# Kernel tuning notes

Measured on AMD Instinct MI355X. Metric: run time of the kernel, lower is better.

Reference implementation:

```python
import jax, jax.numpy as jnp
import numpy as np
from jax import lax

B, T = 8192, 4096


def setup_inputs() -> dict:
    key = jax.random.key(0)
    ks = jax.random.split(key, 16)
    P = jax.random.uniform(ks[0], (B, T, 1), dtype=jnp.float32) * 10.0  # precipitation, mm
    lengths = jax.random.randint(ks[1], (B,), 1, T + 1, dtype=jnp.int32)
    initial_S = jax.random.uniform(ks[2], (4,), dtype=jnp.float32) * 20.0  # initial tank levels
    Area = jnp.array([100.0], dtype=jnp.float32)  # catchment area km^2
    baseflow = jnp.array([0.0], dtype=jnp.float32)  # unused by forward, kept for signature fidelity

    def u(k, lo, hi):
        return jax.random.uniform(k, (1,), dtype=jnp.float32) * (hi - lo) + lo

    params = {
        "outflow_rate_1_h1": u(ks[3], 0.05, 0.25),
        "outflow_rate_1_h2": u(ks[4], 0.05, 0.10),
        "height_1_h1": u(ks[5], 40.0, 60.0),
        "height_1_h2": u(ks[6], 0.0, 40.0),
        "inflow_rate_2": u(ks[7], 0.01, 0.30),
        "outflow_rate_2": u(ks[8], 0.005, 0.30),
        "height_2": u(ks[9], 0.0, 30.0),
        "inflow_rate_3": u(ks[10], 0.005, 0.20),
        "outflow_rate_3": u(ks[11], 0.005, 0.15),
        "height_3": u(ks[12], 0.0, 30.0),
        "inflow_rate_4": u(ks[13], 0.005, 0.10),
        "outflow_rate_4": u(ks[14], 0.0006, 0.10),
    }
    return {"P": P, "lengths": lengths, "initial_S": initial_S, "Area": Area,
            "baseflow": baseflow, **params}


def reference(P, lengths, initial_S, Area, baseflow,
              outflow_rate_1_h1, outflow_rate_1_h2, height_1_h1, height_1_h2,
              inflow_rate_2, outflow_rate_2, height_2,
              inflow_rate_3, outflow_rate_3, height_3,
              inflow_rate_4, outflow_rate_4):
    Pq = P[..., 0]                              # [B, T]
    b, t = Pq.shape
    # valid_mask[b, t] = (lengths[b] > t), as in pad_packed_sequence masking
    mask = (jnp.arange(t)[None, :] < lengths[:, None]).astype(Pq.dtype)  # [B, T]
    w_init = tuple(jnp.broadcast_to(initial_S[i], (b,)) for i in range(4))

    def step(carry, xs):
        w1, w2, w3, w4 = carry
        p, m = xs                               # [B] each
        # Tank 1: two side outlets + bottom percolation into tank 2
        of1h1 = jnp.maximum(outflow_rate_1_h1 * (w1 - height_1_h1 + p), 0.0) * m
        of1h2 = jnp.maximum(outflow_rate_1_h2 * (w1 - height_1_h2 + p), 0.0) * m
        of1 = (of1h1 + of1h2) * m
        out12 = jnp.maximum(inflow_rate_2 * (w1 + p), 0.0) * m
        w1 = w1 + (p - of1 - out12) * m
        # Tank 2
        of2 = jnp.maximum(outflow_rate_2 * (w2 + out12 - height_2), 0.0) * m
        out23 = jnp.maximum(inflow_rate_3 * (w2 + out12), 0.0) * m
        w2 = w2 + (out12 - of2 - out23) * m
        # Tank 3
        of3 = jnp.maximum(outflow_rate_3 * (w3 + out23 - height_3), 0.0) * m
        out34 = jnp.maximum(inflow_rate_4 * (w3 + out23), 0.0) * m
        w3 = w3 + (out23 - of3 - out34) * m
        # Tank 4 (deep baseflow tank)
        of4 = jnp.maximum(outflow_rate_4 * (w4 + out34), 0.0) * m
        w4 = w4 + (out34 - of4) * m
        total = (of1 + of2 + of3 + of4) * m
        return (w1, w2, w3, w4), total * Area / 3.6   # mm -> m^3/s conversion

    _, ys = lax.scan(step, w_init, (Pq.T, mask.T))    # ys: [T, B]
    return ys.T                                        # [B, T]
```

## Files before the change

kernel.cpp:

```cpp
#include <hip/hip_runtime.h>
#include <stdint.h>


__device__ __forceinline__ float quad_rot1(float x) {
    int xi = __builtin_bit_cast(int, x);
    int r = __builtin_amdgcn_update_dpp(xi, xi, 0x93, 0xF, 0xF, false);
    return __builtin_bit_cast(float, r);
}

__global__ __launch_bounds__(64)
void tank_kernel(
    const float* __restrict__ P,
    const int*   __restrict__ lengths,
    const float* __restrict__ S0,
    const float* __restrict__ AreaP,
    const float* __restrict__ p_r1h1, const float* __restrict__ p_r1h2,
    const float* __restrict__ p_h1h1, const float* __restrict__ p_h1h2,
    const float* __restrict__ p_ri2,  const float* __restrict__ p_ro2,
    const float* __restrict__ p_h2,
    const float* __restrict__ p_ri3,  const float* __restrict__ p_ro3,
    const float* __restrict__ p_h3,
    const float* __restrict__ p_ri4,  const float* __restrict__ p_ro4,
    float* __restrict__ Out,
    int B, int T)
{
    __shared__ float4 inbuf[2 * 256];
    __shared__ float4 outbuf[3 * 256];

    const int tid = threadIdx.x;
    const int g   = tid >> 2;
    const int k   = tid & 3;
    const int row = blockIdx.x * 16 + g;
    const int rowc = (row < B) ? row : (B - 1);
    const bool is0 = (k == 0);
    const bool is3 = (k == 3);
    const float zk = (k == 0) ? 0.0f : 1.0f;

    const float v_r1h1 = p_r1h1[0], v_r1h2 = p_r1h2[0];
    const float v_h11 = p_h1h1[0], v_h12 = p_h1h2[0];
    const float v_ri2 = p_ri2[0], v_ro2 = p_ro2[0], v_h2 = p_h2[0];
    const float v_ri3 = p_ri3[0], v_ro3 = p_ro3[0], v_h3 = p_h3[0];
    const float v_ri4 = p_ri4[0], v_ro4 = p_ro4[0];
    const float scale = AreaP[0] * (1.0f / 3.6f);

    float rA = v_ro4, kA = 0.0f, rB = 0.0f, kB = 0.0f, riN = 0.0f;
    if (k == 0) { rA = v_r1h1; kA = -v_r1h1 * v_h11; rB = v_r1h2; kB = -v_r1h2 * v_h12; riN = v_ri2; }
    else if (k == 1) { rA = v_ro2; kA = -v_ro2 * v_h2; riN = v_ri3; }
    else if (k == 2) { rA = v_ro3; kA = -v_ro3 * v_h3; riN = v_ri4; }

    float w = (k == 0) ? S0[0] : (k == 1) ? S0[1] : (k == 2) ? S0[2] : S0[3];

    int len = lengths[rowc];
    if (len > T) len = T;
    if (len < 0) len = 0;

    float fl0 = 0.0f, fl1 = 0.0f, fl2 = 0.0f, fl3 = 0.0f;
    float ps0 = 0.0f, ps1 = 0.0f, ps2 = 0.0f, ps3 = 0.0f;
    const int ntiles = T / 64;

#define HOP4(CX, CY, CZ, CW, FREEZE, hidx) do {                   \
        float r0_ = quad_rot1(fl0);                               \
        float r1_ = quad_rot1(fl1);                               \
        float r2_ = quad_rot1(fl2);                               \
        float r3_ = quad_rot1(fl3);                               \
        float q0_ = quad_rot1(ps0);                               \
        float q1_ = quad_rot1(ps1);                               \
        float q2_ = quad_rot1(ps2);                               \
        float q3_ = quad_rot1(ps3);                               \
        float i0_ = is0 ? (CX) : r0_;                             \
        float i1_ = is0 ? (CY) : r1_;                             \
        float i2_ = is0 ? (CZ) : r2_;                             \
        float i3_ = is0 ? (CW) : r3_;                             \
        float t_, a1_, a2_, e_, Y_, wn_;                          \
                                                      \
        t_  = w + i0_;                                            \
        a1_ = fmaxf(fmaf(rA, t_, kA), 0.0f);                      \
        a2_ = fmaxf(fmaf(rB, t_, kB), 0.0f);                      \
        e_  = fmaxf(t_, 0.0f);                                    \
        fl0 = riN * e_;                                           \
        Y_  = a1_ + a2_;                                          \
        wn_ = (t_ - fl0) - Y_;                                    \
        w = (FREEZE) ? (((hidx) >= k) ? wn_ : w) : wn_;           \
        ps0 = fmaf(q0_, zk, Y_);                                  \
                                                      \
        t_  = w + i1_;                                            \
        a1_ = fmaxf(fmaf(rA, t_, kA), 0.0f);                      \
        a2_ = fmaxf(fmaf(rB, t_, kB), 0.0f);                      \
        e_  = fmaxf(t_, 0.0f);                                    \
        fl1 = riN * e_;                                           \
        Y_  = a1_ + a2_;                                          \
        wn_ = (t_ - fl1) - Y_;                                    \
        w = (FREEZE) ? (((hidx) >= k) ? wn_ : w) : wn_;           \
        ps1 = fmaf(q1_, zk, Y_);                                  \
                                                      \
        t_  = w + i2_;                                            \
        a1_ = fmaxf(fmaf(rA, t_, kA), 0.0f);                      \
        a2_ = fmaxf(fmaf(rB, t_, kB), 0.0f);                      \
        e_  = fmaxf(t_, 0.0f);                                    \
        fl2 = riN * e_;                                           \
        Y_  = a1_ + a2_;                                          \
        wn_ = (t_ - fl2) - Y_;                                    \
        w = (FREEZE) ? (((hidx) >= k) ? wn_ : w) : wn_;           \
        ps2 = fmaf(q2_, zk, Y_);                                  \
                                                      \
        t_  = w + i3_;                                            \
        a1_ = fmaxf(fmaf(rA, t_, kA), 0.0f);                      \
        a2_ = fmaxf(fmaf(rB, t_, kB), 0.0f);                      \
        e_  = fmaxf(t_, 0.0f);                                    \
        fl3 = riN * e_;                                           \
        Y_  = a1_ + a2_;                                          \
        wn_ = (t_ - fl3) - Y_;                                    \
        w = (FREEZE) ? (((hidx) >= k) ? wn_ : w) : wn_;           \
        ps3 = fmaf(q3_, zk, Y_);                                  \
    } while (0)

#define STAGE_LOAD(mt) do {                                               \
        const float* src_ = P + (size_t)rowc * T + (mt) * 64;             \
        _Pragma("unroll")                                                 \
        for (int r = 0; r < 4; ++r)                                       \
            st[r] = *reinterpret_cast<const float4*>(src_ + (4 * r + k) * 4); \
    } while (0)

#define STAGE_LDS(ibp) do {                                  \
        _Pragma("unroll")                                    \
        for (int r = 0; r < 4; ++r)                          \
            (ibp)[g * 16 + ((4 * r + k) ^ g)] = st[r];       \
    } while (0)

#define OUT_STORE(mt) do {                                                \
        const float4* ob_ = outbuf + ((mt) % 3) * 256;                    \
        const int col0_ = (mt) * 64;                                      \
        _Pragma("unroll")                                                 \
        for (int r = 0; r < 4; ++r) {                                     \
            float4 v_ = ob_[g * 16 + ((4 * r + k) ^ g)];                  \
            const int cb_ = col0_ + (4 * r + k) * 4;                      \
            float4 s_;                                                    \
            s_.x = (cb_ + 0 < len) ? v_.x * scale : 0.0f;                 \
            s_.y = (cb_ + 1 < len) ? v_.y * scale : 0.0f;                 \
            s_.z = (cb_ + 2 < len) ? v_.z * scale : 0.0f;                 \
            s_.w = (cb_ + 3 < len) ? v_.w * scale : 0.0f;                 \
            if (row < B)                                                  \
                *reinterpret_cast<float4*>(Out + (size_t)row * T + cb_) = s_; \
        }                                                                 \
    } while (0)

#define TILE_BODY(FREEZE, h0, ibp) do {                                   \
        float4 c0 = (ibp)[g * 16 + (0 ^ g)];                              \
        float4 c1 = (ibp)[g * 16 + (1 ^ g)];                              \
        _Pragma("unroll 4")                                               \
        for (int j4 = 0; j4 < 16; ++j4) {                                 \
            float4 c2 = (ibp)[g * 16 + (((j4 + 2) & 15) ^ g)];            \
            HOP4(c0.x, c0.y, c0.z, c0.w, FREEZE, j4);                     \
            const int b_ = (h0) + j4 - 3;                                 \
            if ((!(FREEZE) || b_ >= 0) && is3) {                          \
                float4* obp_ = outbuf + ((b_ >> 4) % 3) * 256;            \
                obp_[g * 16 + ((b_ & 15) ^ g)] =                          \
                    make_float4(ps0, ps1, ps2, ps3);                      \
            }                                                             \
            c0 = c1; c1 = c2;                                             \
        }                                                                 \
    } while (0)

    float4 st[4];
    STAGE_LOAD(0);
    STAGE_LDS(inbuf);
    __syncthreads();
    if (ntiles > 1) STAGE_LOAD(1);
    TILE_BODY(1, 0, inbuf);

    for (int m = 1; m < ntiles; ++m) {
        float4* ib = inbuf + (m & 1) * 256;
        STAGE_LDS(ib);
        __syncthreads();
        if (m >= 2) OUT_STORE(m - 2);
        if (m + 1 < ntiles) STAGE_LOAD(m + 1);
        TILE_BODY(0, m * 16, ib);
    }

    {
        const int nb = T >> 2;
        #pragma unroll
        for (int d = 0; d < 3; ++d) {
            HOP4(0.0f, 0.0f, 0.0f, 0.0f, 0, 0);
            const int b_ = nb - 3 + d;
            if (is3) {
                float4* obp = outbuf + ((b_ >> 4) % 3) * 256;
                obp[g * 16 + ((b_ & 15) ^ g)] = make_float4(ps0, ps1, ps2, ps3);
            }
        }
    }
#undef HOP4
#undef TILE_BODY

    __syncthreads();
    OUT_STORE(ntiles - 2);
    OUT_STORE(ntiles - 1);
#undef OUT_STORE
#undef STAGE_LOAD
#undef STAGE_LDS
}

extern "C" void kernel_launch(void* const* d_in, const int* in_sizes, int n_in,
                              void* d_out, int out_size, void* d_ws, size_t ws_size,
                              hipStream_t stream) {
    const float* P        = (const float*)d_in[0];
    const int*   lengths  = (const int*)d_in[1];
    const float* S0       = (const float*)d_in[2];
    const float* Area     = (const float*)d_in[3];
    const float* r1h1 = (const float*)d_in[5];
    const float* r1h2 = (const float*)d_in[6];
    const float* h1h1 = (const float*)d_in[7];
    const float* h1h2 = (const float*)d_in[8];
    const float* ri2  = (const float*)d_in[9];
    const float* ro2  = (const float*)d_in[10];
    const float* h2   = (const float*)d_in[11];
    const float* ri3  = (const float*)d_in[12];
    const float* ro3  = (const float*)d_in[13];
    const float* h3   = (const float*)d_in[14];
    const float* ri4  = (const float*)d_in[15];
    const float* ro4  = (const float*)d_in[16];
    float* out = (float*)d_out;

    const int B = in_sizes[1];
    const int T = in_sizes[0] / B;

    dim3 block(64);
    dim3 grid((B + 15) / 16);
    hipLaunchKernelGGL(tank_kernel, grid, block, 0, stream,
                       P, lengths, S0, Area,
                       r1h1, r1h2, h1h1, h1h2,
                       ri2, ro2, h2, ri3, ro3, h3, ri4, ro4,
                       out, B, T);
}
```

Baseline: 439.7 us.

## Replace LDS input staging with register double-buffer and DPP quad broadcasts

Precipitation tiles are no longer written to and re-read from shared memory. Each lane keeps its loaded float4s in one of two register buffers (stA/stB), and the value needed at each step is shared across the 4-lane quad with DPP broadcasts. This removes the LDS input buffer and the per-tile __syncthreads; the block is a single 64-thread wave, so the output LDS buffer stays ordered without a barrier. The main loop is manually unrolled by two tiles with a tail tile, which assumes an even tile count and adds register pressure from the full unroll.

Result: faster. 379.4 us (-13.7%).

```diff
diff --git a/kernel.cpp b/kernel.cpp
--- a/kernel.cpp
+++ b/kernel.cpp
@@ -5,6 +5,18 @@
 __device__ __forceinline__ float quad_rot1(float x) {
     int xi = __builtin_bit_cast(int, x);
     int r = __builtin_amdgcn_update_dpp(xi, xi, 0x93, 0xF, 0xF, false);
+    return __builtin_bit_cast(float, r);
+}
+
+__device__ __forceinline__ float quad_bcast(float x, int s) {
+    int xi = __builtin_bit_cast(int, x);
+    int r;
+    switch (s & 3) {
+    case 0:  r = __builtin_amdgcn_update_dpp(xi, xi, 0x00, 0xF, 0xF, false); break;
+    case 1:  r = __builtin_amdgcn_update_dpp(xi, xi, 0x55, 0xF, 0xF, false); break;
+    case 2:  r = __builtin_amdgcn_update_dpp(xi, xi, 0xAA, 0xF, 0xF, false); break;
+    default: r = __builtin_amdgcn_update_dpp(xi, xi, 0xFF, 0xF, 0xF, false); break;
+    }
     return __builtin_bit_cast(float, r);
 }
 
@@ -24,7 +36,6 @@
     float* __restrict__ Out,
     int B, int T)
 {
-    __shared__ float4 inbuf[2 * 256];
     __shared__ float4 outbuf[3 * 256];
 
     const int tid = threadIdx.x;
@@ -114,17 +125,11 @@
         ps3 = fmaf(q3_, zk, Y_);                                  \
     } while (0)
 
-#define STAGE_LOAD(mt) do {                                               \
+#define STAGE_LOAD(stN, mt) do {                                          \
         const float* src_ = P + (size_t)rowc * T + (mt) * 64;             \
         _Pragma("unroll")                                                 \
         for (int r = 0; r < 4; ++r)                                       \
-            st[r] = *reinterpret_cast<const float4*>(src_ + (4 * r + k) * 4); \
-    } while (0)
-
-#define STAGE_LDS(ibp) do {                                  \
-        _Pragma("unroll")                                    \
-        for (int r = 0; r < 4; ++r)                          \
-            (ibp)[g * 16 + ((4 * r + k) ^ g)] = st[r];       \
+            stN[r] = *reinterpret_cast<const float4*>(src_ + (4 * r + k) * 4); \
     } while (0)
 
 #define OUT_STORE(mt) do {                                                \
@@ -144,38 +149,41 @@
         }                                                                 \
     } while (0)
 
-#define TILE_BODY(FREEZE, h0, ibp) do {                                   \
-        float4 c0 = (ibp)[g * 16 + (0 ^ g)];                              \
-        float4 c1 = (ibp)[g * 16 + (1 ^ g)];                              \
-        _Pragma("unroll 4")                                               \
+#define TILE_BODY(FREEZE, h0, stN) do {                                   \
+        _Pragma("unroll")                                                 \
         for (int j4 = 0; j4 < 16; ++j4) {                                 \
-            float4 c2 = (ibp)[g * 16 + (((j4 + 2) & 15) ^ g)];            \
-            HOP4(c0.x, c0.y, c0.z, c0.w, FREEZE, j4);                     \
+            const float4 pv_ = stN[j4 >> 2];                              \
+            float px_ = quad_bcast(pv_.x, j4);                            \
+            float py_ = quad_bcast(pv_.y, j4);                            \
+            float pz_ = quad_bcast(pv_.z, j4);                            \
+            float pw_ = quad_bcast(pv_.w, j4);                            \
+            HOP4(px_, py_, pz_, pw_, FREEZE, j4);                         \
             const int b_ = (h0) + j4 - 3;                                 \
             if ((!(FREEZE) || b_ >= 0) && is3) {                          \
                 float4* obp_ = outbuf + ((b_ >> 4) % 3) * 256;            \
                 obp_[g * 16 + ((b_ & 15) ^ g)] =                          \
                     make_float4(ps0, ps1, ps2, ps3);                      \
             }                                                             \
-            c0 = c1; c1 = c2;                                             \
         }                                                                 \
     } while (0)
 
-    float4 st[4];
-    STAGE_LOAD(0);
-    STAGE_LDS(inbuf);
-    __syncthreads();
-    if (ntiles > 1) STAGE_LOAD(1);
-    TILE_BODY(1, 0, inbuf);
-
-    for (int m = 1; m < ntiles; ++m) {
-        float4* ib = inbuf + (m & 1) * 256;
-        STAGE_LDS(ib);
-        __syncthreads();
-        if (m >= 2) OUT_STORE(m - 2);
-        if (m + 1 < ntiles) STAGE_LOAD(m + 1);
-        TILE_BODY(0, m * 16, ib);
+    float4 stA[4], stB[4];
+    STAGE_LOAD(stA, 0);
+    if (ntiles > 1) STAGE_LOAD(stB, 1);
+    TILE_BODY(1, 0, stA);
+
+    #pragma clang loop unroll(disable)
+    for (int m = 1; m + 1 < ntiles; m += 2) {
+        STAGE_LOAD(stA, m + 1);
+        if (m >= 3) OUT_STORE(m - 2);
+        TILE_BODY(0, m * 16, stB);
+        STAGE_LOAD(stB, m + 2);
+        OUT_STORE(m - 1);
+        TILE_BODY(0, (m + 1) * 16, stA);
     }
+
+    OUT_STORE(ntiles - 3);
+    TILE_BODY(0, (ntiles - 1) * 16, stB);
 
     {
         const int nb = T >> 2;
@@ -192,12 +200,10 @@
 #undef HOP4
 #undef TILE_BODY
 
-    __syncthreads();
     OUT_STORE(ntiles - 2);
     OUT_STORE(ntiles - 1);
 #undef OUT_STORE
 #undef STAGE_LOAD
-#undef STAGE_LDS
 }
 
 extern "C" void kernel_launch(void* const* d_in, const int* in_sizes, int n_in,
```
